# Performance work log

Hardware: AMD Instinct MI355X
Metric: run time of the kernel (lower is better)

The kernel has to match this reference:

```python
import jax, jax.numpy as jnp
import numpy as np

N, NFEAT, NHID, NCLASS, NHEADS = 4096, 512, 64, 16, 8
ALPHA = 0.2  # LeakyReLU negative slope


def setup_inputs() -> dict:
    key = jax.random.key(0)
    ks = jax.random.split(key, 5)
    return {
        "x": jax.random.normal(ks[0], (N, NFEAT), jnp.float32),
        "Wh": jax.random.normal(ks[1], (NHEADS, NFEAT, NHID), jnp.float32) * 0.05,
        "ah": jax.random.normal(ks[2], (NHEADS, 2 * NHID), jnp.float32) * 0.1,
        "Wo": jax.random.normal(ks[3], (NHEADS * NHID, NCLASS), jnp.float32) * 0.05,
        "ao": jax.random.normal(ks[4], (2 * NCLASS,), jnp.float32) * 0.1,
    }


def _gat_layer(x, W, a, concat):
    # h = x W  [N, F]
    h = x @ W
    F = h.shape[-1]
    # additive score decomposes: e_ij = leakyrelu(h_i . a[:F] + h_j . a[F:])
    s_src = h @ a[:F]  # [N]
    s_dst = h @ a[F:]  # [N]
    e = jax.nn.leaky_relu(s_src[:, None] + s_dst[None, :], ALPHA)  # [N, N]
    att = jax.nn.softmax(e, axis=1)
    feat = att @ h  # [N, F]
    return jax.nn.elu(feat) if concat else feat


def reference(x, Wh, ah, Wo, ao):
    # multi-head layers, concatenated along features (head-major order, as torch cat)
    heads = jax.vmap(lambda W, a: _gat_layer(x, W, a, True))(Wh, ah)  # [H, N, nhid]
    xc = jnp.transpose(heads, (1, 0, 2)).reshape(x.shape[0], -1)  # [N, H*nhid]
    out = jax.nn.elu(_gat_layer(xc, Wo, ao, False))  # [N, nclass]
    return jax.nn.log_softmax(out, axis=1)
```

## Files before the change

kernel.cpp:

```cpp
#include <hip/hip_runtime.h>
#include <math.h>

#define N 4096
#define NFEAT 512
#define NHID 64
#define NCLASS 16
#define NHEADS 8
#define ALPHA 0.2f
#define JSPL 8
#define JLEN (N / JSPL)
#define HSTR 520
#define J1 256
#define H1STR 264

typedef __attribute__((ext_vector_type(8))) short bf16x8;
typedef __attribute__((ext_vector_type(4))) float f32x4;

__device__ inline unsigned short f2bf(float f) {
  unsigned u = __float_as_uint(f);
  unsigned r = u + 0x7fffu + ((u >> 16) & 1u);
  return (unsigned short)(r >> 16);
}
__device__ inline unsigned mono(float f) {
  unsigned u = __float_as_uint(f);
  return (u & 0x80000000u) ? ~u : (u | 0x80000000u);
}
__device__ inline float unmono(unsigned m) {
  return (m >> 31) ? __uint_as_float(m & 0x7FFFFFFFu) : __uint_as_float(~m);
}

__global__ __launch_bounds__(256) void k_pack(const float* __restrict__ x,
                                              const float* __restrict__ Wh,
                                              const float* __restrict__ Wo,
                                              unsigned short* __restrict__ xb,
                                              unsigned short* __restrict__ Wt,
                                              unsigned short* __restrict__ Wt2,
                                              unsigned* __restrict__ tmax1u,
                                              unsigned* __restrict__ tmax2u) {
  int b = blockIdx.x;
  if (b < 2048) {
    int i = (b * 256 + threadIdx.x) * 4;
    float4 v = *(const float4*)(x + i);
    ushort4 o;
    o.x = f2bf(v.x); o.y = f2bf(v.y); o.z = f2bf(v.z); o.w = f2bf(v.w);
    *(ushort4*)(xb + i) = o;
  } else if (b < 2112) {
    int idx = b - 2048;
    int kt = idx & 7, hd = idx >> 3;
    __shared__ float ld[64][65];
    const float* src = Wh + ((size_t)hd * NFEAT + kt * 64) * NHID;
    int r = threadIdx.x >> 2, c0 = (threadIdx.x & 3) * 16;
#pragma unroll
    for (int j = 0; j < 4; ++j) {
      float4 v = *(const float4*)(src + (size_t)r * NHID + c0 + j * 4);
      ld[r][c0 + j * 4 + 0] = v.x; ld[r][c0 + j * 4 + 1] = v.y;
      ld[r][c0 + j * 4 + 2] = v.z; ld[r][c0 + j * 4 + 3] = v.w;
    }
    __syncthreads();
    int n = threadIdx.x >> 2, kq = threadIdx.x & 3;
    unsigned short tmp[16];
#pragma unroll
    for (int j = 0; j < 16; ++j) tmp[j] = f2bf(ld[kq * 16 + j][n]);
    unsigned short* dst = Wt + ((size_t)hd * 64 + n) * NFEAT + kt * 64 + kq * 16;
    ((uint4*)dst)[0] = *(uint4*)tmp;
    ((uint4*)dst)[1] = *(uint4*)(tmp + 8);
  } else {
    for (int e = threadIdx.x; e < NFEAT * NCLASS; e += 256) {
      int n = e & 15, k = e >> 4;
      Wt2[(size_t)n * NFEAT + k] = f2bf(Wo[(size_t)k * NCLASS + n]);
    }
    if (threadIdx.x < NHEADS) tmax1u[threadIdx.x] = 0u;
    if (threadIdx.x == 0) *tmax2u = 0u;
  }
}

__global__ __launch_bounds__(256) void k_gemm_h(const unsigned short* __restrict__ xb,
                                                const unsigned short* __restrict__ Wt,
                                                const float* __restrict__ ah,
                                                unsigned short* __restrict__ h1T,
                                                float* __restrict__ ssrc,
                                                float* __restrict__ sdst,
                                                unsigned* __restrict__ tmax1u) {
  const int hd = blockIdx.y;
  const int i0 = blockIdx.x * 128;
  const int t = threadIdx.x;
  const int w = t >> 6, lane = t & 63;
  const int lr = lane & 15, kg = lane >> 4;
  const int wm = (w & 1) * 64, wn = (w >> 1) * 32;
  __shared__ uint4 Als[128][4];
  __shared__ uint4 Bls[64][4];
  __shared__ float sredS[128][2];
  __shared__ float sredD[128][2];
  const unsigned short* xrow = xb + (size_t)i0 * NFEAT;
  const unsigned short* wrow = Wt + (size_t)hd * 64 * NFEAT;

  f32x4 acc[4][2];
#pragma unroll
  for (int a = 0; a < 4; ++a)
#pragma unroll
    for (int b = 0; b < 2; ++b) acc[a][b] = (f32x4){0.f, 0.f, 0.f, 0.f};

  const int u0 = t, u1 = t + 256;
  const int ra0 = u0 >> 2, sa0 = ((u0 & 3) ^ (ra0 & 3)) * 8;
  const int ra1 = u1 >> 2, sa1 = ((u1 & 3) ^ (ra1 & 3)) * 8;
  const int rb0 = t >> 2,  sb0 = ((t & 3) ^ (rb0 & 3)) * 8;
  const int wbase = t & ~63;

  for (int k0 = 0; k0 < NFEAT; k0 += 32) {
    __builtin_amdgcn_global_load_lds(
        (const __attribute__((address_space(1))) void*)(xrow + (size_t)ra0 * NFEAT + k0 + sa0),
        (__attribute__((address_space(3))) void*)((uint4*)Als + wbase), 16, 0, 0);
    __builtin_amdgcn_global_load_lds(
        (const __attribute__((address_space(1))) void*)(xrow + (size_t)ra1 * NFEAT + k0 + sa1),
        (__attribute__((address_space(3))) void*)((uint4*)Als + 256 + wbase), 16, 0, 0);
    __builtin_amdgcn_global_load_lds(
        (const __attribute__((address_space(1))) void*)(wrow + (size_t)rb0 * NFEAT + k0 + sb0),
        (__attribute__((address_space(3))) void*)((uint4*)Bls + wbase), 16, 0, 0);
    __syncthreads();
    bf16x8 af[4], bfv[2];
#pragma unroll
    for (int mb = 0; mb < 4; ++mb) {
      int row = wm + mb * 16 + lr;
      af[mb] = __builtin_bit_cast(bf16x8, Als[row][kg ^ (row & 3)]);
    }
#pragma unroll
    for (int nb = 0; nb < 2; ++nb) {
      int col = wn + nb * 16 + lr;
      bfv[nb] = __builtin_bit_cast(bf16x8, Bls[col][kg ^ (col & 3)]);
    }
#pragma unroll
    for (int mb = 0; mb < 4; ++mb)
#pragma unroll
      for (int nb = 0; nb < 2; ++nb)
        acc[mb][nb] = __builtin_amdgcn_mfma_f32_16x16x32_bf16(af[mb], bfv[nb], acc[mb][nb], 0, 0, 0);
    __syncthreads();
  }

  unsigned short* hT = h1T + (size_t)hd * NHID * N;
#pragma unroll
  for (int mb = 0; mb < 4; ++mb)
#pragma unroll
    for (int nb = 0; nb < 2; ++nb) {
      int col = wn + nb * 16 + lr;
      int rbase = i0 + wm + mb * 16 + kg * 4;
      ushort4 o;
      o.x = f2bf(acc[mb][nb][0]); o.y = f2bf(acc[mb][nb][1]);
      o.z = f2bf(acc[mb][nb][2]); o.w = f2bf(acc[mb][nb][3]);
      *(ushort4*)(hT + (size_t)col * N + rbase) = o;
    }

  float aS[2], aD[2];
#pragma unroll
  for (int nb = 0; nb < 2; ++nb) {
    aS[nb] = ah[hd * 128 + wn + nb * 16 + lr];
    aD[nb] = ah[hd * 128 + 64 + wn + nb * 16 + lr];
  }
#pragma unroll
  for (int mb = 0; mb < 4; ++mb)
#pragma unroll
    for (int reg = 0; reg < 4; ++reg) {
      float ps = acc[mb][0][reg] * aS[0] + acc[mb][1][reg] * aS[1];
      float pd = acc[mb][0][reg] * aD[0] + acc[mb][1][reg] * aD[1];
#pragma unroll
      for (int m = 1; m < 16; m <<= 1) { ps += __shfl_xor(ps, m); pd += __shfl_xor(pd, m); }
      if (lr == 0) {
        int rl = wm + mb * 16 + kg * 4 + reg;
        sredS[rl][w >> 1] = ps;
        sredD[rl][w >> 1] = pd;
      }
    }
  __syncthreads();
  if (t < 128) {
    float vs = sredS[t][0] + sredS[t][1];
    float vd = sredD[t][0] + sredD[t][1];
    ssrc[(size_t)hd * N + i0 + t] = vs;
    sdst[(size_t)hd * N + i0 + t] = vd;
    float m = vd;
#pragma unroll
    for (int mk = 32; mk; mk >>= 1) m = fmaxf(m, __shfl_xor(m, mk));
    if ((t & 63) == 0) atomicMax(tmax1u + hd, mono(m));
  }
}

__global__ __launch_bounds__(256) void k_attn1(const float* __restrict__ ssrc,
                                               const float* __restrict__ sdst,
                                               const unsigned short* __restrict__ h1T,
                                               const unsigned* __restrict__ tmax1u,
                                               unsigned short* __restrict__ xcb) {
  __shared__ float tl[J1];
  __shared__ unsigned short hsT[64 * H1STR];
  const int hd = blockIdx.y;
  const int tid = threadIdx.x, w = tid >> 6, lane = tid & 63;
  const int lr = lane & 15, kg = lane >> 4;
  const int row16 = blockIdx.x * 64 + w * 16;
  const unsigned short* hTh = h1T + (size_t)hd * NHID * N;
  const float* th = sdst + (size_t)hd * N;
  float tmax = unmono(tmax1u[hd]);
  float s = ssrc[(size_t)hd * N + row16 + lr];
  float v0 = s + tmax;
  float rowm = fmaxf(v0, ALPHA * v0);
  f32x4 acc[4];
#pragma unroll
  for (int nb = 0; nb < 4; ++nb) acc[nb] = (f32x4){0.f, 0.f, 0.f, 0.f};
  float zpart = 0.f;

  for (int jc = 0; jc < N / J1; ++jc) {
    if (tid < 64) *(float4*)(tl + tid * 4) = *(const float4*)(th + jc * J1 + tid * 4);
#pragma unroll
    for (int rep = 0; rep < 8; ++rep) {
      int u = rep * 256 + tid;
      int r = u >> 5, cu = u & 31;
      *(uint4*)(hsT + r * H1STR + cu * 8) =
          *(const uint4*)(hTh + (size_t)r * N + jc * J1 + cu * 8);
    }
    __syncthreads();
#pragma unroll
    for (int c = 0; c < J1 / 32; ++c) {
      const float* tp = tl + c * 32 + kg * 8;
      float e[8];
#pragma unroll
      for (int m = 0; m < 8; ++m) {
        float v = s + tp[m];
        e[m] = __expf(fmaxf(v, ALPHA * v) - rowm);
        zpart += e[m];
      }
      unsigned pk[4];
#pragma unroll
      for (int p = 0; p < 4; ++p)
        pk[p] = ((unsigned)f2bf(e[2 * p + 1]) << 16) | (unsigned)f2bf(e[2 * p]);
      bf16x8 af = __builtin_bit_cast(bf16x8, *(uint4*)pk);
#pragma unroll
      for (int nb = 0; nb < 4; ++nb) {
        bf16x8 bf = __builtin_bit_cast(bf16x8,
            *(const uint4*)(hsT + (nb * 16 + lr) * H1STR + c * 32 + kg * 8));
        acc[nb] = __builtin_amdgcn_mfma_f32_16x16x32_bf16(af, bf, acc[nb], 0, 0, 0);
      }
    }
    __syncthreads();
  }
  zpart += __shfl_xor(zpart, 16);
  zpart += __shfl_xor(zpart, 32);
#pragma unroll
  for (int reg = 0; reg < 4; ++reg) {
    float rz = 1.f / __shfl(zpart, kg * 4 + reg);
    int row = row16 + kg * 4 + reg;
#pragma unroll
    for (int nb = 0; nb < 4; ++nb) {
      float f = acc[nb][reg] * rz;
      float e2 = f > 0.f ? f : expf(f) - 1.f;
      xcb[(size_t)row * (NHEADS * NHID) + hd * NHID + nb * 16 + lr] = f2bf(e2);
    }
  }
}

__global__ __launch_bounds__(256) void k_gemm2(const unsigned short* __restrict__ xcb,
                                               const unsigned short* __restrict__ Wt2,
                                               const float* __restrict__ ao,
                                               unsigned short* __restrict__ h2b,
                                               float* __restrict__ ssrc,
                                               float* __restrict__ sdst,
                                               unsigned* __restrict__ tmax2u) {
  const int t = threadIdx.x;
  const int w = t >> 6, lane = t & 63;
  const int lr = lane & 15, kg = lane >> 4;
  const int i0 = blockIdx.x * 64 + w * 16;
  __shared__ float sd[64];
  f32x4 acc = (f32x4){0.f, 0.f, 0.f, 0.f};
  const unsigned short* arow = xcb + (size_t)(i0 + lr) * NFEAT;
  const unsigned short* brow = Wt2 + (size_t)lr * NFEAT;
#pragma unroll
  for (int k0 = 0; k0 < NFEAT; k0 += 32) {
    bf16x8 af = __builtin_bit_cast(bf16x8, *(const uint4*)(arow + k0 + kg * 8));
    bf16x8 bv = __builtin_bit_cast(bf16x8, *(const uint4*)(brow + k0 + kg * 8));
    acc = __builtin_amdgcn_mfma_f32_16x16x32_bf16(af, bv, acc, 0, 0, 0);
  }
  float aS = ao[lr], aD = ao[16 + lr];
#pragma unroll
  for (int reg = 0; reg < 4; ++reg) {
    int row = i0 + kg * 4 + reg;
    h2b[(size_t)row * NCLASS + lr] = f2bf(acc[reg]);
    float ps = acc[reg] * aS, pd = acc[reg] * aD;
#pragma unroll
    for (int m = 1; m < 16; m <<= 1) { ps += __shfl_xor(ps, m); pd += __shfl_xor(pd, m); }
    if (lr == 0) {
      ssrc[row] = ps;
      sdst[row] = pd;
      sd[w * 16 + kg * 4 + reg] = pd;
    }
  }
  __syncthreads();
  if (t < 64) {
    float v = sd[t];
#pragma unroll
    for (int m = 32; m; m >>= 1) v = fmaxf(v, __shfl_xor(v, m));
    if (t == 0) atomicMax(tmax2u, mono(v));
  }
}

__global__ __launch_bounds__(256) void k_attn2p(const float* __restrict__ ssrc,
                                                const float* __restrict__ t,
                                                const unsigned short* __restrict__ h2b,
                                                const unsigned* __restrict__ tmax2u,
                                                float* __restrict__ pnum,
                                                float* __restrict__ pz) {
  __shared__ float tl[JLEN];
  __shared__ unsigned short hsT[16 * HSTR];
  int tid = threadIdx.x;
  int jb = blockIdx.y;
  if (tid < 128) {
    int i4 = tid * 4;
    *(float4*)(tl + i4) = *(const float4*)(t + jb * JLEN + i4);
  }
#pragma unroll
  for (int rep = 0; rep < 2; ++rep) {
    int j = rep * 256 + tid;
    const uint4* src = (const uint4*)(h2b + (size_t)(jb * JLEN + j) * NCLASS);
    uint4 a = src[0], b = src[1];
    unsigned short v[16];
    *(uint4*)v = a; *(uint4*)(v + 8) = b;
#pragma unroll
    for (int c = 0; c < 16; ++c) hsT[c * HSTR + j] = v[c];
  }
  __syncthreads();
  int w = tid >> 6, lane = tid & 63;
  int lr = lane & 15, kg = lane >> 4;
  int ib = blockIdx.x * 64 + w * 16;
  float tmax = unmono(*tmax2u);
  float s = ssrc[ib + lr];
  float v0 = s + tmax;
  float rowm = fmaxf(v0, ALPHA * v0);
  f32x4 acc = (f32x4){0.f, 0.f, 0.f, 0.f};
  float zpart = 0.f;
#pragma unroll
  for (int c = 0; c < JLEN / 32; ++c) {
    const float* tp = tl + c * 32 + kg * 8;
    float e[8];
#pragma unroll
    for (int m = 0; m < 8; ++m) {
      float v = s + tp[m];
      e[m] = __expf(fmaxf(v, ALPHA * v) - rowm);
      zpart += e[m];
    }
    unsigned pk[4];
#pragma unroll
    for (int p = 0; p < 4; ++p)
      pk[p] = ((unsigned)f2bf(e[2 * p + 1]) << 16) | (unsigned)f2bf(e[2 * p]);
    bf16x8 af = __builtin_bit_cast(bf16x8, *(uint4*)pk);
    bf16x8 bf = __builtin_bit_cast(bf16x8,
        *(const uint4*)(hsT + lr * HSTR + c * 32 + kg * 8));
    acc = __builtin_amdgcn_mfma_f32_16x16x32_bf16(af, bf, acc, 0, 0, 0);
  }
  zpart += __shfl_xor(zpart, 16);
  zpart += __shfl_xor(zpart, 32);
#pragma unroll
  for (int reg = 0; reg < 4; ++reg)
    pnum[((size_t)jb * N + ib + kg * 4 + reg) * NCLASS + lr] = acc[reg];
  if (lane < 16) pz[(size_t)jb * N + ib + lane] = zpart;
}

__global__ __launch_bounds__(256) void k_attn2f(const float* __restrict__ pnum,
                                                const float* __restrict__ pz,
                                                float* __restrict__ out) {
  int g = threadIdx.x >> 4, cl = threadIdx.x & 15;
  int i = blockIdx.x * 16 + g;
  float nsum = 0.f, zsum = 0.f;
#pragma unroll
  for (int jb = 0; jb < JSPL; ++jb) {
    nsum += pnum[((size_t)jb * N + i) * NCLASS + cl];
    zsum += pz[(size_t)jb * N + i];
  }
  float o = nsum / zsum;
  o = o > 0.f ? o : expf(o) - 1.f;
  float mo = o;
#pragma unroll
  for (int mk = 1; mk < 16; mk <<= 1) mo = fmaxf(mo, __shfl_xor(mo, mk, 16));
  float sum = expf(o - mo);
#pragma unroll
  for (int mk = 1; mk < 16; mk <<= 1) sum += __shfl_xor(sum, mk, 16);
  out[(size_t)i * NCLASS + cl] = o - mo - logf(sum);
}

extern "C" void kernel_launch(void* const* d_in, const int* in_sizes, int n_in,
                              void* d_out, int out_size, void* d_ws, size_t ws_size,
                              hipStream_t stream) {
  const float* x  = (const float*)d_in[0];
  const float* Wh = (const float*)d_in[1];
  const float* ah = (const float*)d_in[2];
  const float* Wo = (const float*)d_in[3];
  const float* ao = (const float*)d_in[4];
  float* out = (float*)d_out;

  char* base = (char*)d_ws;
  size_t off = 0;
  auto alloc_f = [&](size_t n) -> float* {
    float* p = (float*)(base + off);
    off = (off + n * sizeof(float) + 255) & ~(size_t)255;
    return p;
  };
  auto alloc_i = [&](size_t n) -> int* {
    int* p = (int*)(base + off);
    off = (off + n * sizeof(int) + 255) & ~(size_t)255;
    return p;
  };
  auto alloc_u16 = [&](size_t n) -> unsigned short* {
    unsigned short* p = (unsigned short*)(base + off);
    off = (off + n * sizeof(unsigned short) + 255) & ~(size_t)255;
    return p;
  };

  unsigned short* xbf = alloc_u16((size_t)N * NFEAT);
  unsigned short* Wt  = alloc_u16((size_t)NHEADS * NHID * NFEAT);
  unsigned short* Wt2 = alloc_u16((size_t)NCLASS * NFEAT);
  unsigned short* h1T = alloc_u16((size_t)NHEADS * NHID * N);
  float* ssrc1 = alloc_f((size_t)NHEADS * N);
  float* sdst1 = alloc_f((size_t)NHEADS * N);
  unsigned* tmax1u = (unsigned*)alloc_i(NHEADS);
  unsigned short* xcb = alloc_u16((size_t)N * NHEADS * NHID);
  unsigned short* h2b = alloc_u16((size_t)N * NCLASS);
  float* ssrc2 = alloc_f(N);
  float* sdst2 = alloc_f(N);
  unsigned* tmax2u = (unsigned*)alloc_i(1);
  float* pnum  = alloc_f((size_t)JSPL * N * NCLASS);
  float* pz    = alloc_f((size_t)JSPL * N);

  if (off > ws_size) return;

  hipLaunchKernelGGL(k_pack, dim3(2113), dim3(256), 0, stream, x, Wh, Wo, xbf, Wt, Wt2, tmax1u, tmax2u);

  hipLaunchKernelGGL(k_gemm_h, dim3(N / 128, NHEADS), dim3(256), 0, stream, xbf, Wt, ah, h1T, ssrc1, sdst1, tmax1u);
  hipLaunchKernelGGL(k_attn1, dim3(N / 64, NHEADS), dim3(256), 0, stream, ssrc1, sdst1, h1T, tmax1u, xcb);

  hipLaunchKernelGGL(k_gemm2, dim3(N / 64), dim3(256), 0, stream, xcb, Wt2, ao, h2b, ssrc2, sdst2, tmax2u);
  hipLaunchKernelGGL(k_attn2p, dim3(N / 64, JSPL), dim3(256), 0, stream, ssrc2, sdst2, h2b, tmax2u, pnum, pz);
  hipLaunchKernelGGL(k_attn2f, dim3(N / 16), dim3(256), 0, stream, pnum, pz, out);
}
```

Measured before the change: 106.0 us.

## Process two row tiles per wave in attn1 with XOR-swizzled LDS and truncating bf16 pack

Each wave in the first-layer attention kernel now handles 32 rows instead of 16, so every h^T fragment loaded from LDS feeds two MFMAs. The block count is halved, which halves the global-to-LDS traffic for h1T per head. The LDS tile drops its padding and uses an XOR swizzle on 16-byte chunks to avoid bank conflicts. The bf16 conversion of attention weights now truncates instead of rounding to nearest, which saves ALU work but adds a small precision loss. The cost is more registers per thread and half as many blocks (256), which lowers occupancy.

Result: slower. 150.8 us (+42.3%).

```diff
diff --git a/kernel.cpp b/kernel.cpp
--- a/kernel.cpp
+++ b/kernel.cpp
@@ -11,7 +11,6 @@
 #define JLEN (N / JSPL)
 #define HSTR 520
 #define J1 256
-#define H1STR 264
 
 typedef __attribute__((ext_vector_type(8))) short bf16x8;
 typedef __attribute__((ext_vector_type(4))) float f32x4;
@@ -188,21 +187,26 @@
                                                const unsigned* __restrict__ tmax1u,
                                                unsigned short* __restrict__ xcb) {
   __shared__ float tl[J1];
-  __shared__ unsigned short hsT[64 * H1STR];
+  __shared__ unsigned short hsT[64 * 256];
   const int hd = blockIdx.y;
   const int tid = threadIdx.x, w = tid >> 6, lane = tid & 63;
   const int lr = lane & 15, kg = lane >> 4;
-  const int row16 = blockIdx.x * 64 + w * 16;
+  const int row32 = blockIdx.x * 128 + w * 32;
   const unsigned short* hTh = h1T + (size_t)hd * NHID * N;
   const float* th = sdst + (size_t)hd * N;
   float tmax = unmono(tmax1u[hd]);
-  float s = ssrc[(size_t)hd * N + row16 + lr];
-  float v0 = s + tmax;
-  float rowm = fmaxf(v0, ALPHA * v0);
-  f32x4 acc[4];
-#pragma unroll
-  for (int nb = 0; nb < 4; ++nb) acc[nb] = (f32x4){0.f, 0.f, 0.f, 0.f};
-  float zpart = 0.f;
+  float sA = ssrc[(size_t)hd * N + row32 + lr];
+  float sB = ssrc[(size_t)hd * N + row32 + 16 + lr];
+  float vA0 = sA + tmax, vB0 = sB + tmax;
+  float rowmA = fmaxf(vA0, ALPHA * vA0);
+  float rowmB = fmaxf(vB0, ALPHA * vB0);
+  f32x4 accA[4], accB[4];
+#pragma unroll
+  for (int nb = 0; nb < 4; ++nb) {
+    accA[nb] = (f32x4){0.f, 0.f, 0.f, 0.f};
+    accB[nb] = (f32x4){0.f, 0.f, 0.f, 0.f};
+  }
+  float zA = 0.f, zB = 0.f;
 
   for (int jc = 0; jc < N / J1; ++jc) {
     if (tid < 64) *(float4*)(tl + tid * 4) = *(const float4*)(th + jc * J1 + tid * 4);
@@ -210,45 +214,60 @@
     for (int rep = 0; rep < 8; ++rep) {
       int u = rep * 256 + tid;
       int r = u >> 5, cu = u & 31;
-      *(uint4*)(hsT + r * H1STR + cu * 8) =
+      int pcu = cu ^ (r & 7);
+      *(uint4*)(hsT + r * 256 + pcu * 8) =
           *(const uint4*)(hTh + (size_t)r * N + jc * J1 + cu * 8);
     }
     __syncthreads();
 #pragma unroll
     for (int c = 0; c < J1 / 32; ++c) {
       const float* tp = tl + c * 32 + kg * 8;
-      float e[8];
+      float eA[8], eB[8];
 #pragma unroll
       for (int m = 0; m < 8; ++m) {
-        float v = s + tp[m];
-        e[m] = __expf(fmaxf(v, ALPHA * v) - rowm);
-        zpart += e[m];
+        float tj = tp[m];
+        float vA = sA + tj, vB = sB + tj;
+        eA[m] = __expf(fmaxf(vA, ALPHA * vA) - rowmA);
+        eB[m] = __expf(fmaxf(vB, ALPHA * vB) - rowmB);
+        zA += eA[m]; zB += eB[m];
       }
-      unsigned pk[4];
-#pragma unroll
-      for (int p = 0; p < 4; ++p)
-        pk[p] = ((unsigned)f2bf(e[2 * p + 1]) << 16) | (unsigned)f2bf(e[2 * p]);
-      bf16x8 af = __builtin_bit_cast(bf16x8, *(uint4*)pk);
+      unsigned pkA[4], pkB[4];
+#pragma unroll
+      for (int p = 0; p < 4; ++p) {
+        pkA[p] = (__float_as_uint(eA[2 * p + 1]) & 0xFFFF0000u) |
+                 (__float_as_uint(eA[2 * p]) >> 16);
+        pkB[p] = (__float_as_uint(eB[2 * p + 1]) & 0xFFFF0000u) |
+                 (__float_as_uint(eB[2 * p]) >> 16);
+      }
+      bf16x8 afA = __builtin_bit_cast(bf16x8, *(uint4*)pkA);
+      bf16x8 afB = __builtin_bit_cast(bf16x8, *(uint4*)pkB);
+      int pu = (c * 4 + kg) ^ (lr & 7);
 #pragma unroll
       for (int nb = 0; nb < 4; ++nb) {
-        bf16x8 bf = __builtin_bit_cast(bf16x8,
-            *(const uint4*)(hsT + (nb * 16 + lr) * H1STR + c * 32 + kg * 8));
-        acc[nb] = __builtin_amdgcn_mfma_f32_16x16x32_bf16(af, bf, acc[nb], 0, 0, 0);
+        bf16x8 bfv = __builtin_bit_cast(bf16x8,
+            *(const uint4*)(hsT + (nb * 16 + lr) * 256 + pu * 8));
+        accA[nb] = __builtin_amdgcn_mfma_f32_16x16x32_bf16(afA, bfv, accA[nb], 0, 0, 0);
+        accB[nb] = __builtin_amdgcn_mfma_f32_16x16x32_bf16(afB, bfv, accB[nb], 0, 0, 0);
       }
     }
     __syncthreads();
   }
-  zpart += __shfl_xor(zpart, 16);
-  zpart += __shfl_xor(zpart, 32);
+  zA += __shfl_xor(zA, 16); zA += __shfl_xor(zA, 32);
+  zB += __shfl_xor(zB, 16); zB += __shfl_xor(zB, 32);
 #pragma unroll
   for (int reg = 0; reg < 4; ++reg) {
-    float rz = 1.f / __shfl(zpart, kg * 4 + reg);
-    int row = row16 + kg * 4 + reg;
+    int rsel = kg * 4 + reg;
+    float rzA = 1.f / __shfl(zA, rsel);
+    float rzB = 1.f / __shfl(zB, rsel);
+    int rowA = row32 + rsel, rowB = row32 + 16 + rsel;
 #pragma unroll
     for (int nb = 0; nb < 4; ++nb) {
-      float f = acc[nb][reg] * rz;
-      float e2 = f > 0.f ? f : expf(f) - 1.f;
-      xcb[(size_t)row * (NHEADS * NHID) + hd * NHID + nb * 16 + lr] = f2bf(e2);
+      float fA = accA[nb][reg] * rzA;
+      float fB = accB[nb][reg] * rzB;
+      float gA = fA > 0.f ? fA : expf(fA) - 1.f;
+      float gB = fB > 0.f ? fB : expf(fB) - 1.f;
+      xcb[(size_t)rowA * (NHEADS * NHID) + hd * NHID + nb * 16 + lr] = f2bf(gA);
+      xcb[(size_t)rowB * (NHEADS * NHID) + hd * NHID + nb * 16 + lr] = f2bf(gB);
     }
   }
 }
@@ -428,7 +447,7 @@
   hipLaunchKernelGGL(k_pack, dim3(2113), dim3(256), 0, stream, x, Wh, Wo, xbf, Wt, Wt2, tmax1u, tmax2u);
 
   hipLaunchKernelGGL(k_gemm_h, dim3(N / 128, NHEADS), dim3(256), 0, stream, xbf, Wt, ah, h1T, ssrc1, sdst1, tmax1u);
-  hipLaunchKernelGGL(k_attn1, dim3(N / 64, NHEADS), dim3(256), 0, stream, ssrc1, sdst1, h1T, tmax1u, xcb);
+  hipLaunchKernelGGL(k_attn1, dim3(N / 128, NHEADS), dim3(256), 0, stream, ssrc1, sdst1, h1T, tmax1u, xcb);
 
   hipLaunchKernelGGL(k_gemm2, dim3(N / 64), dim3(256), 0, stream, xcb, Wt2, ao, h2b, ssrc2, sdst2, tmax2u);
   hipLaunchKernelGGL(k_attn2p, dim3(N / 64, JSPL), dim3(256), 0, stream, ssrc2, sdst2, h2b, tmax2u, pnum, pz);
```

## Split first-layer attention over two key halves with a separate reduction kernel

Applied to the files above, without the earlier changes.

The first-layer attention kernel now splits the key dimension into two halves, doubling the grid from 512 to 1024 blocks. Each block writes unnormalized fp32 partial numerators and partition sums to a workspace. A new finalize kernel adds the partials, normalizes, applies ELU and writes the bf16 concatenated features. This is meant to give the 256 CUs more blocks to run at once. It costs an extra launch and about 16 MB of fp32 partial traffic written and read back.

Result: no change. 104.4 us (-1.5%).

```diff
diff --git a/kernel.cpp b/kernel.cpp
--- a/kernel.cpp
+++ b/kernel.cpp
@@ -12,6 +12,7 @@
 #define HSTR 520
 #define J1 256
 #define H1STR 264
+#define JSPL1 2
 
 typedef __attribute__((ext_vector_type(8))) short bf16x8;
 typedef __attribute__((ext_vector_type(4))) float f32x4;
@@ -186,10 +187,12 @@
                                                const float* __restrict__ sdst,
                                                const unsigned short* __restrict__ h1T,
                                                const unsigned* __restrict__ tmax1u,
-                                               unsigned short* __restrict__ xcb) {
+                                               float* __restrict__ pnum1,
+                                               float* __restrict__ pz1) {
   __shared__ float tl[J1];
   __shared__ unsigned short hsT[64 * H1STR];
-  const int hd = blockIdx.y;
+  const int hd = blockIdx.y >> 1;
+  const int jb = blockIdx.y & 1;
   const int tid = threadIdx.x, w = tid >> 6, lane = tid & 63;
   const int lr = lane & 15, kg = lane >> 4;
   const int row16 = blockIdx.x * 64 + w * 16;
@@ -204,7 +207,8 @@
   for (int nb = 0; nb < 4; ++nb) acc[nb] = (f32x4){0.f, 0.f, 0.f, 0.f};
   float zpart = 0.f;
 
-  for (int jc = 0; jc < N / J1; ++jc) {
+  const int jc0 = jb * (N / J1 / JSPL1);
+  for (int jc = jc0; jc < jc0 + N / J1 / JSPL1; ++jc) {
     if (tid < 64) *(float4*)(tl + tid * 4) = *(const float4*)(th + jc * J1 + tid * 4);
 #pragma unroll
     for (int rep = 0; rep < 8; ++rep) {
@@ -240,17 +244,33 @@
   }
   zpart += __shfl_xor(zpart, 16);
   zpart += __shfl_xor(zpart, 32);
+  float* pn = pnum1 + ((size_t)(jb * NHEADS + hd) * N) * NHID;
 #pragma unroll
   for (int reg = 0; reg < 4; ++reg) {
-    float rz = 1.f / __shfl(zpart, kg * 4 + reg);
     int row = row16 + kg * 4 + reg;
 #pragma unroll
-    for (int nb = 0; nb < 4; ++nb) {
-      float f = acc[nb][reg] * rz;
-      float e2 = f > 0.f ? f : expf(f) - 1.f;
-      xcb[(size_t)row * (NHEADS * NHID) + hd * NHID + nb * 16 + lr] = f2bf(e2);
-    }
-  }
+    for (int nb = 0; nb < 4; ++nb)
+      pn[(size_t)row * NHID + nb * 16 + lr] = acc[nb][reg];
+  }
+  if (lane < 16)
+    pz1[(size_t)(jb * NHEADS + hd) * N + row16 + lane] = zpart;
+}
+
+__global__ __launch_bounds__(256) void k_attn1f(const float* __restrict__ pnum1,
+                                                const float* __restrict__ pz1,
+                                                unsigned short* __restrict__ xcb) {
+  int hd = blockIdx.y;
+  int w = threadIdx.x >> 6, lane = threadIdx.x & 63;
+  int row = blockIdx.x * 4 + w;
+  float nsum = 0.f, zsum = 0.f;
+#pragma unroll
+  for (int jb = 0; jb < JSPL1; ++jb) {
+    nsum += pnum1[((size_t)(jb * NHEADS + hd) * N + row) * NHID + lane];
+    zsum += pz1[(size_t)(jb * NHEADS + hd) * N + row];
+  }
+  float f = nsum / zsum;
+  float e = f > 0.f ? f : expf(f) - 1.f;
+  xcb[(size_t)row * (NHEADS * NHID) + hd * NHID + lane] = f2bf(e);
 }
 
 __global__ __launch_bounds__(256) void k_gemm2(const unsigned short* __restrict__ xcb,
@@ -415,6 +435,8 @@
   float* ssrc1 = alloc_f((size_t)NHEADS * N);
   float* sdst1 = alloc_f((size_t)NHEADS * N);
   unsigned* tmax1u = (unsigned*)alloc_i(NHEADS);
+  float* pnum1 = alloc_f((size_t)JSPL1 * NHEADS * N * NHID);
+  float* pz1   = alloc_f((size_t)JSPL1 * NHEADS * N);
   unsigned short* xcb = alloc_u16((size_t)N * NHEADS * NHID);
   unsigned short* h2b = alloc_u16((size_t)N * NCLASS);
   float* ssrc2 = alloc_f(N);
@@ -428,7 +450,8 @@
   hipLaunchKernelGGL(k_pack, dim3(2113), dim3(256), 0, stream, x, Wh, Wo, xbf, Wt, Wt2, tmax1u, tmax2u);
 
   hipLaunchKernelGGL(k_gemm_h, dim3(N / 128, NHEADS), dim3(256), 0, stream, xbf, Wt, ah, h1T, ssrc1, sdst1, tmax1u);
-  hipLaunchKernelGGL(k_attn1, dim3(N / 64, NHEADS), dim3(256), 0, stream, ssrc1, sdst1, h1T, tmax1u, xcb);
+  hipLaunchKernelGGL(k_attn1, dim3(N / 64, NHEADS * JSPL1), dim3(256), 0, stream, ssrc1, sdst1, h1T, tmax1u, pnum1, pz1);
+  hipLaunchKernelGGL(k_attn1f, dim3(N / 4, NHEADS), dim3(256), 0, stream, pnum1, pz1, xcb);
 
   hipLaunchKernelGGL(k_gemm2, dim3(N / 64), dim3(256), 0, stream, xcb, Wt2, ao, h2b, ssrc2, sdst2, tmax2u);
   hipLaunchKernelGGL(k_attn2p, dim3(N / 64, JSPL), dim3(256), 0, stream, ssrc2, sdst2, h2b, tmax2u, pnum, pz);
```
